# Optimization experiments

Hardware: AMD Instinct MI355X
Metric: run time of the kernel (lower is better)

The kernel has to match this reference:

```python
import jax, jax.numpy as jnp
import numpy as np

N_NODES = 50000
N_EDGES = 800000
N_GRAPHS = 512
NEG_SLOPE = 0.2  # PyG GATConv default LeakyReLU slope


def _gat_layer(x, src, dst, W, a_src, a_dst, b, n_nodes):
    """PyG-style GATConv (concat=True, self-loops already in src/dst)."""
    H, C = a_src.shape
    h = (x @ W).reshape(n_nodes, H, C)            # [N, H, C]
    e_s = (h * a_src).sum(-1)                     # [N, H]
    e_d = (h * a_dst).sum(-1)                     # [N, H]
    e = jax.nn.leaky_relu(e_s[src] + e_d[dst], NEG_SLOPE)  # [E, H]
    # segment softmax over destination nodes
    m = jax.ops.segment_max(e, dst, num_segments=n_nodes)
    w = jnp.exp(e - m[dst])
    s = jax.ops.segment_sum(w, dst, num_segments=n_nodes)
    alpha = w / (s[dst] + 1e-16)                  # [E, H]
    out = jax.ops.segment_sum(h[src] * alpha[:, :, None], dst, num_segments=n_nodes)
    return out.reshape(n_nodes, H * C) + b


def setup_inputs() -> dict:
    key = jax.random.key(0)
    ks = jax.random.split(key, 16)
    x = jax.random.normal(ks[0], (N_NODES, 2), dtype=jnp.float32)
    edge_index = jax.random.randint(ks[1], (2, N_EDGES), 0, N_NODES, dtype=jnp.int64 if jax.config.jax_enable_x64 else jnp.int32)
    batch = jnp.sort(jax.random.randint(ks[2], (N_NODES,), 0, N_GRAPHS))
    g = lambda k, shape: (jax.random.normal(k, shape, dtype=jnp.float32) * 0.1)
    return {
        "x": x, "edge_index": edge_index, "batch": batch,
        "W1": g(ks[3], (2, 64)),   "a1s": g(ks[4], (8, 8)),  "a1d": g(ks[5], (8, 8)),  "b1": jnp.zeros((64,), jnp.float32),
        "W2": g(ks[6], (64, 128)), "a2s": g(ks[7], (8, 16)), "a2d": g(ks[8], (8, 16)), "b2": jnp.zeros((128,), jnp.float32),
        "W3": g(ks[9], (128, 128)),"a3s": g(ks[10], (8, 16)),"a3d": g(ks[11], (8, 16)),"b3": jnp.zeros((128,), jnp.float32),
        "fc1W": g(ks[12], (128, 32)), "fc1b": jnp.zeros((32,), jnp.float32),
        "fc2W": g(ks[13], (32, 10)),  "fc2b": jnp.zeros((10,), jnp.float32),
    }


def reference(x, edge_index, batch, W1, a1s, a1d, b1, W2, a2s, a2d, b2, W3, a3s, a3d, b3, fc1W, fc1b, fc2W, fc2b):
    n = x.shape[0]
    loop = jnp.arange(n, dtype=edge_index.dtype)
    src = jnp.concatenate([edge_index[0], loop])  # add self-loops (PyG default)
    dst = jnp.concatenate([edge_index[1], loop])
    h = jax.nn.elu(_gat_layer(x, src, dst, W1, a1s, a1d, b1, n))
    h = jax.nn.elu(_gat_layer(h, src, dst, W2, a2s, a2d, b2, n))
    h = _gat_layer(h, src, dst, W3, a3s, a3d, b3, n)
    # global mean pool over graphs
    sums = jax.ops.segment_sum(h, batch, num_segments=N_GRAPHS)
    cnt = jax.ops.segment_sum(jnp.ones((n,), h.dtype), batch, num_segments=N_GRAPHS)
    pooled = sums / jnp.maximum(cnt, 1.0)[:, None]   # [G, 128]
    z = jax.nn.relu(pooled @ fc1W + fc1b)
    return jax.nn.log_softmax(z @ fc2W + fc2b, axis=1)
```

## Files before the change

### kernel.cpp

```cpp
#include <hip/hip_runtime.h>
#include <cstddef>
#include <cstdint>

typedef __attribute__((ext_vector_type(8))) short bf16x8;
typedef __attribute__((ext_vector_type(4))) float floatx4;
typedef __attribute__((ext_vector_type(2))) float v2f;

#define BSTRIDE 8192


__device__ __forceinline__ unsigned bf16pair(float a, float b) {
    unsigned ua = __float_as_uint(a), ub = __float_as_uint(b);
    ua += 0x7fffu + ((ua >> 16) & 1u);
    ub += 0x7fffu + ((ub >> 16) & 1u);
    return (ua >> 16) | (ub & 0xffff0000u);
}
__device__ __forceinline__ unsigned short bf16one(float a) {
    unsigned ua = __float_as_uint(a);
    ua += 0x7fffu + ((ua >> 16) & 1u);
    return (unsigned short)(ua >> 16);
}


__global__ __launch_bounds__(256) void prep_k(
    const int* __restrict__ edge, unsigned* __restrict__ barr,
    int* __restrict__ bcnt, int E, int EA, int B1,
    const float* __restrict__ W2, unsigned short* __restrict__ Wt2,
    const float* __restrict__ W3, unsigned short* __restrict__ Wt3,
    const float* __restrict__ x, const float* __restrict__ W1,
    const float* __restrict__ a1s, const float* __restrict__ a1d,
    unsigned char* __restrict__ h8a, float* __restrict__ es,
    float* __restrict__ ed, int N) {
    int tid = threadIdx.x;
    if ((int)blockIdx.x < B1) {
        __shared__ int h[256];
        __shared__ int lbase[256];
        h[tid] = 0;
        __syncthreads();
        int start = blockIdx.x * 4096;
        unsigned ent[16];
        int lp[16];
#pragma unroll
        for (int k = 0; k < 16; ++k) {
            int i = start + k * 256 + tid;
            if (i < EA) {
                int s, d;
                if (i < E) { s = edge[i]; d = edge[E + i]; }
                else { s = i - E; d = s; }
                int b = d >> 8;
                ent[k] = (unsigned)s | ((unsigned)(d & 255) << 16) | ((unsigned)b << 24);
                lp[k] = atomicAdd(&h[b], 1);
            } else {
                ent[k] = 0xffffffffu;
                lp[k] = 0;
            }
        }
        __syncthreads();
        lbase[tid] = h[tid] ? atomicAdd(&bcnt[tid], h[tid]) : 0;
        __syncthreads();
#pragma unroll
        for (int k = 0; k < 16; ++k) {
            if (ent[k] != 0xffffffffu) {
                int b = ent[k] >> 24;
                int pos = lbase[b] + lp[k];
                if (pos < BSTRIDE)
                    barr[(size_t)b * BSTRIDE + pos] = ent[k] & 0x00ffffffu;
            }
        }
        return;
    }
    if ((int)blockIdx.x < B1 + 96) {
        int rel = blockIdx.x - B1;
        const float* W = (rel < 32) ? W2 : W3;
        unsigned short* Wt = (rel < 32) ? Wt2 : Wt3;
        int total = (rel < 32) ? 8192 : 16384;
        int o = ((rel < 32) ? rel : rel - 32) * 256 + tid;
        if (o < total) {
            int j = o & 7, lane = (o >> 3) & 63, ct = (o >> 9) & 7, ks = o >> 12;
            int k = ks * 32 + (lane >> 4) * 8 + j;
            int n = ct * 16 + (lane & 15);
            Wt[o] = bf16one(W[k * 128 + n]);
        }
        return;
    }
    int wave = tid >> 6, lane = tid & 63;
    int nbase = (blockIdx.x - B1 - 96) * 32;
    float w0 = W1[lane], w1 = W1[64 + lane];
    float as = a1s[lane], ad = a1d[lane];
    int head = lane >> 3;
#pragma unroll
    for (int it = 0; it < 8; ++it) {
        int n = nbase + it * 4 + wave;
        int nc = (n < N) ? n : N - 1;
        float2 xv = ((const float2*)x)[nc];
        float h = xv.x * w0 + xv.y * w1;
        float ps = h * as, pd = h * ad;
#pragma unroll
        for (int off = 1; off < 8; off <<= 1) {
            ps += __shfl_xor(ps, off);
            pd += __shfl_xor(pd, off);
        }
        if (n < N) {
            unsigned d = __builtin_amdgcn_cvt_pk_fp8_f32(h, h, 0, false);
            h8a[(size_t)n * 64 + lane] = (unsigned char)d;
            if ((lane & 7) == 0) { es[n * 8 + head] = ps; ed[n * 8 + head] = pd; }
        }
    }
}


__global__ __launch_bounds__(256) void bucket2_k(const unsigned* __restrict__ barr,
                                                 const int* __restrict__ bcnt,
                                                 int* __restrict__ offsets,
                                                 int* __restrict__ esrc,
                                                 int N, int EA, int nbuck) {
    __shared__ int sd[256];
    __shared__ int bb[256];
    __shared__ int cur[256];
    int b = blockIdx.x, tid = threadIdx.x;
    int v = (tid < nbuck) ? bcnt[tid] : 0;
    sd[tid] = v;
    __syncthreads();
    for (int off = 1; off < 256; off <<= 1) {
        int t = (tid >= off) ? sd[tid - off] : 0;
        __syncthreads();
        sd[tid] += t;
        __syncthreads();
    }
    bb[tid] = sd[tid] - v;
    __syncthreads();
    int bbase = bb[b];
    if (b == 0 && tid == 0) offsets[N] = EA;
    if (b == 0 && tid < 8) esrc[EA + tid] = 0;

    int cnt = bcnt[b];
    const unsigned* arr = barr + (size_t)b * BSTRIDE;
    sd[tid] = 0;
    __syncthreads();
    for (int i = tid; i < cnt; i += 256)
        atomicAdd(&sd[(arr[i] >> 16) & 0xff], 1);
    __syncthreads();
    v = sd[tid];
    for (int off = 1; off < 256; off <<= 1) {
        int t = (tid >= off) ? sd[tid - off] : 0;
        __syncthreads();
        sd[tid] += t;
        __syncthreads();
    }
    int base = bbase + sd[tid] - v;
    int n = b * 256 + tid;
    if (n < N) offsets[n] = base;
    cur[tid] = base;
    __syncthreads();
    for (int i = tid; i < cnt; i += 256) {
        unsigned e = arr[i];
        int pos = atomicAdd(&cur[(e >> 16) & 0xff], 1);
        esrc[pos] = (int)(e & 0xffffu);
    }
}


template <int IN>
__global__ __launch_bounds__(256) void gemm_mfma_k(
    const unsigned short* __restrict__ a16, const unsigned short* __restrict__ Wt,
    const float* __restrict__ a_s, const float* __restrict__ a_d,
    unsigned char* __restrict__ h8, float* __restrict__ es, float* __restrict__ ed,
    int n_nodes) {
    constexpr int KSTEPS = IN / 32;
    __shared__ float Cl[64 * 132];
    int wave = threadIdx.x >> 6, lane = threadIdx.x & 63;
    int q = lane >> 4, m = lane & 15;
    int rbase = blockIdx.x * 64;

    floatx4 acc[8];
#pragma unroll
    for (int ct = 0; ct < 8; ++ct) acc[ct] = (floatx4){0.f, 0.f, 0.f, 0.f};

    int ra = rbase + wave * 16 + m;
    if (ra >= n_nodes) ra = n_nodes - 1;
    const unsigned short* arow = a16 + (size_t)ra * IN + q * 8;

#pragma unroll
    for (int ks = 0; ks < KSTEPS; ++ks) {
        bf16x8 af = *(const bf16x8*)(arow + ks * 32);
        const unsigned short* wp = Wt + ((size_t)(ks * 8) * 64 + lane) * 8;
#pragma unroll
        for (int ct = 0; ct < 8; ++ct) {
            bf16x8 bf = *(const bf16x8*)(wp + (size_t)ct * 64 * 8);
            acc[ct] = __builtin_amdgcn_mfma_f32_16x16x32_bf16(af, bf, acc[ct], 0, 0, 0);
        }
    }

#pragma unroll
    for (int ct = 0; ct < 8; ++ct)
#pragma unroll
        for (int i = 0; i < 4; ++i)
            Cl[(wave * 16 + q * 4 + i) * 132 + ct * 16 + m] = acc[ct][i];
    __syncthreads();

    int rl = threadIdx.x >> 2, part = threadIdx.x & 3;
    int r = rbase + rl;
    if (r < n_nodes) {
        const float* cp = &Cl[rl * 132 + part * 32];
        float e0s = 0.f, e0d = 0.f, e1s = 0.f, e1d = 0.f;
#pragma unroll
        for (int c = 0; c < 16; ++c) {
            float v = cp[c];
            int ai = part * 32 + c;
            e0s += v * a_s[ai];
            e0d += v * a_d[ai];
        }
#pragma unroll
        for (int c = 16; c < 32; ++c) {
            float v = cp[c];
            int ai = part * 32 + c;
            e1s += v * a_s[ai];
            e1d += v * a_d[ai];
        }
        unsigned pk8[8];
#pragma unroll
        for (int u = 0; u < 8; ++u) {
            unsigned d = __builtin_amdgcn_cvt_pk_fp8_f32(cp[4 * u], cp[4 * u + 1], 0, false);
            d = __builtin_amdgcn_cvt_pk_fp8_f32(cp[4 * u + 2], cp[4 * u + 3], d, true);
            pk8[u] = d;
        }
        uint4* hp = (uint4*)(h8 + (size_t)r * 128) + part * 2;
        hp[0] = make_uint4(pk8[0], pk8[1], pk8[2], pk8[3]);
        hp[1] = make_uint4(pk8[4], pk8[5], pk8[6], pk8[7]);
        es[r * 8 + 2 * part] = e0s;
        es[r * 8 + 2 * part + 1] = e1s;
        ed[r * 8 + 2 * part] = e0d;
        ed[r * 8 + 2 * part + 1] = e1d;
    }
}


template <int NCOL, bool ELU, bool POOL>
__global__ __launch_bounds__(256) void gat_k(
    const unsigned char* __restrict__ hsrc, const float* __restrict__ es,
    const float* __restrict__ ed, const int* __restrict__ offsets,
    const int* __restrict__ esrc, const float* __restrict__ bias,
    void* __restrict__ outp, const int* __restrict__ batch,
    float* __restrict__ sums, float* __restrict__ cnt, int n_nodes) {
    constexpr int UPL = NCOL / 16;
    __shared__ float vbuf[POOL ? 8 * 128 : 1];
    int wave = threadIdx.x >> 6, lane = threadIdx.x & 63;
    int half = lane >> 5;
    int hl = lane & 31;
    int slot = hl >> 3;
    int l = lane & 7;
    int ni = wave * 2 + half;
    int n = blockIdx.x * 8 + ni;
    bool valid = (n < n_nodes);
    int nc = valid ? n : 0;
    float edn = ed[nc * 8 + l];
    int start = valid ? offsets[nc] : 0;
    int end = valid ? offsets[nc + 1] : 0;

    v2f acc2[UPL];
#pragma unroll
    for (int k = 0; k < UPL; ++k) acc2[k] = (v2f){0.f, 0.f};
    float s = 0.f;

    for (int j = start; j < end; j += 4) {
        int jj = j + slot;
        bool act = (jj < end);
        int src = esrc[jj];
        float e0 = es[(size_t)src * 8 + l] + edn;
        float e = fmaxf(e0, 0.2f * e0);
        float p = act ? __expf(e) : 0.f;
        s += p;
        v2f p2 = (v2f){p, p};
        if constexpr (NCOL == 128) {
            uint4 u = *(const uint4*)(hsrc + (size_t)src * 128 + 16 * l);
            acc2[0] += p2 * (v2f)__builtin_amdgcn_cvt_pk_f32_fp8(u.x, false);
            acc2[1] += p2 * (v2f)__builtin_amdgcn_cvt_pk_f32_fp8(u.x, true);
            acc2[2] += p2 * (v2f)__builtin_amdgcn_cvt_pk_f32_fp8(u.y, false);
            acc2[3] += p2 * (v2f)__builtin_amdgcn_cvt_pk_f32_fp8(u.y, true);
            acc2[4] += p2 * (v2f)__builtin_amdgcn_cvt_pk_f32_fp8(u.z, false);
            acc2[5] += p2 * (v2f)__builtin_amdgcn_cvt_pk_f32_fp8(u.z, true);
            acc2[6] += p2 * (v2f)__builtin_amdgcn_cvt_pk_f32_fp8(u.w, false);
            acc2[7] += p2 * (v2f)__builtin_amdgcn_cvt_pk_f32_fp8(u.w, true);
        } else {
            uint2 u = *(const uint2*)(hsrc + (size_t)src * 64 + 8 * l);
            acc2[0] += p2 * (v2f)__builtin_amdgcn_cvt_pk_f32_fp8(u.x, false);
            acc2[1] += p2 * (v2f)__builtin_amdgcn_cvt_pk_f32_fp8(u.x, true);
            acc2[2] += p2 * (v2f)__builtin_amdgcn_cvt_pk_f32_fp8(u.y, false);
            acc2[3] += p2 * (v2f)__builtin_amdgcn_cvt_pk_f32_fp8(u.y, true);
        }
    }

    s += __shfl_xor(s, 8);
    s += __shfl_xor(s, 16);
    float v[2 * UPL];
#pragma unroll
    for (int k = 0; k < UPL; ++k) { v[2 * k] = acc2[k].x; v[2 * k + 1] = acc2[k].y; }
#pragma unroll
    for (int k = 0; k < 2 * UPL; ++k) {
        v[k] += __shfl_xor(v[k], 8);
        v[k] += __shfl_xor(v[k], 16);
    }

    if (slot == 0 && valid) {
        float r = 1.f / (s + 1e-16f);
#pragma unroll
        for (int k = 0; k < 2 * UPL; ++k) {
            float b = bias[(2 * UPL) * l + k];
            float t = v[k] * r + b;
            if constexpr (ELU) t = (t > 0.f) ? t : expm1f(t);
            v[k] = t;
        }
        if constexpr (POOL) {
#pragma unroll
            for (int k = 0; k < 2 * UPL; ++k)
                vbuf[ni * 128 + (2 * UPL) * l + k] = v[k];
        } else if constexpr (NCOL == 128) {
            uint4* op = (uint4*)outp + (size_t)n * 16 + 2 * l;
            op[0] = make_uint4(bf16pair(v[0], v[1]), bf16pair(v[2], v[3]),
                               bf16pair(v[4], v[5]), bf16pair(v[6], v[7]));
            op[1] = make_uint4(bf16pair(v[8], v[9]), bf16pair(v[10], v[11]),
                               bf16pair(v[12], v[13]), bf16pair(v[14], v[15]));
        } else {
            ((uint4*)outp)[(size_t)n * 8 + l] =
                make_uint4(bf16pair(v[0], v[1]), bf16pair(v[2], v[3]),
                           bf16pair(v[4], v[5]), bf16pair(v[6], v[7]));
        }
    }

    if constexpr (POOL) {
        __syncthreads();
        int c = threadIdx.x;
        if (c < 128) {
            float acc = 0.f, cacc = 0.f;
            int gprev = -1;
            for (int k = 0; k < 8; ++k) {
                int nn = blockIdx.x * 8 + k;
                if (nn >= n_nodes) break;
                int g = batch[nn];
                if (g != gprev) {
                    if (gprev >= 0) {
                        atomicAdd(&sums[gprev * 128 + c], acc);
                        if (c == 0) atomicAdd(&cnt[gprev], cacc);
                    }
                    acc = 0.f; cacc = 0.f; gprev = g;
                }
                acc += vbuf[k * 128 + c];
                cacc += 1.f;
            }
            if (gprev >= 0) {
                atomicAdd(&sums[gprev * 128 + c], acc);
                if (c == 0) atomicAdd(&cnt[gprev], cacc);
            }
        }
    }
}


__global__ __launch_bounds__(64) void fc_k(const float* __restrict__ sums,
                                           const float* __restrict__ cnt,
                                           const float* __restrict__ fc1W,
                                           const float* __restrict__ fc1b,
                                           const float* __restrict__ fc2W,
                                           const float* __restrict__ fc2b,
                                           float* __restrict__ out) {
    int g = blockIdx.x, lane = threadIdx.x;
    __shared__ float p[128];
    __shared__ float z[32];
    __shared__ float logits[10];
    float inv = 1.f / fmaxf(cnt[g], 1.f);
    p[lane] = sums[g * 128 + lane] * inv;
    p[lane + 64] = sums[g * 128 + 64 + lane] * inv;
    __syncthreads();
    if (lane < 32) {
        float a = fc1b[lane];
        for (int k = 0; k < 128; k++) a += p[k] * fc1W[k * 32 + lane];
        z[lane] = fmaxf(a, 0.f);
    }
    __syncthreads();
    if (lane < 10) {
        float a = fc2b[lane];
        for (int k = 0; k < 32; k++) a += z[k] * fc2W[k * 10 + lane];
        logits[lane] = a;
    }
    __syncthreads();
    if (lane < 10) {
        float mx = logits[0];
#pragma unroll
        for (int i = 1; i < 10; i++) mx = fmaxf(mx, logits[i]);
        float se = 0.f;
#pragma unroll
        for (int i = 0; i < 10; i++) se += __expf(logits[i] - mx);
        out[g * 10 + lane] = logits[lane] - mx - logf(se);
    }
}


extern "C" void kernel_launch(void* const* d_in, const int* in_sizes, int n_in,
                              void* d_out, int out_size, void* d_ws, size_t ws_size,
                              hipStream_t stream) {
    const float* x = (const float*)d_in[0];
    const int* edge = (const int*)d_in[1];
    const int* batch = (const int*)d_in[2];
    const float* W1 = (const float*)d_in[3];
    const float* a1s = (const float*)d_in[4];
    const float* a1d = (const float*)d_in[5];
    const float* b1 = (const float*)d_in[6];
    const float* W2 = (const float*)d_in[7];
    const float* a2s = (const float*)d_in[8];
    const float* a2d = (const float*)d_in[9];
    const float* b2 = (const float*)d_in[10];
    const float* W3 = (const float*)d_in[11];
    const float* a3s = (const float*)d_in[12];
    const float* a3d = (const float*)d_in[13];
    const float* b3 = (const float*)d_in[14];
    const float* fc1W = (const float*)d_in[15];
    const float* fc1b = (const float*)d_in[16];
    const float* fc2W = (const float*)d_in[17];
    const float* fc2b = (const float*)d_in[18];
    float* out = (float*)d_out;

    const int N = in_sizes[0] / 2;
    const int E = in_sizes[1] / 2;
    const int EA = E + N;
    const int NG = out_size / 10;
    const int NBUCK = (N + 255) >> 8;
    const int B1 = (EA + 4095) / 4096;
    const int G1 = (N + 31) / 32;

    char* p = (char*)d_ws;
    unsigned char* h8 = (unsigned char*)p; p += (size_t)N * 128;
    unsigned char* h8a = (unsigned char*)p; p += (size_t)N * 64;
    unsigned short* a16a = (unsigned short*)p; p += (size_t)N * 64 * 2;
    unsigned short* a16b = (unsigned short*)p; p += (size_t)N * 128 * 2;
    unsigned short* Wt2 = (unsigned short*)p; p += (size_t)64 * 128 * 2;
    unsigned short* Wt3 = (unsigned short*)p; p += (size_t)128 * 128 * 2;
    float* es = (float*)p;  p += (size_t)N * 8 * 4;
    float* ed = (float*)p;  p += (size_t)N * 8 * 4;
    float* sums = (float*)p; p += (size_t)NG * 128 * 4;
    float* cnt = (float*)p;  p += (size_t)NG * 4;
    int* bcnt = (int*)p;     p += 256 * 4;
    int* offsets = (int*)p;  p += (size_t)(N + 1) * 4;
    int* esrc = (int*)p;     p += (size_t)(EA + 8) * 4;
    unsigned* barr = (unsigned*)p; p += (size_t)NBUCK * BSTRIDE * 4;

    hipMemsetAsync(sums, 0, ((size_t)NG * 128 + NG + 256) * 4, stream);

    prep_k<<<B1 + 96 + G1, 256, 0, stream>>>(
        edge, barr, bcnt, E, EA, B1, W2, Wt2, W3, Wt3,
        x, W1, a1s, a1d, h8a, es, ed, N);
    bucket2_k<<<NBUCK, 256, 0, stream>>>(barr, bcnt, offsets, esrc, N, EA, NBUCK);

    int mblocks = (N + 63) / 64;
    int ablocks = (N + 7) / 8;
    gat_k<64, true, false><<<ablocks, 256, 0, stream>>>(
        h8a, es, ed, offsets, esrc, b1, a16a, batch, sums, cnt, N);
    gemm_mfma_k<64><<<mblocks, 256, 0, stream>>>(a16a, Wt2, a2s, a2d, h8, es, ed, N);
    gat_k<128, true, false><<<ablocks, 256, 0, stream>>>(
        h8, es, ed, offsets, esrc, b2, a16b, batch, sums, cnt, N);
    gemm_mfma_k<128><<<mblocks, 256, 0, stream>>>(a16b, Wt3, a3s, a3d, h8, es, ed, N);
    gat_k<128, false, true><<<ablocks, 256, 0, stream>>>(
        h8, es, ed, offsets, esrc, b3, nullptr, batch, sums, cnt, N);

    fc_k<<<NG, 64, 0, stream>>>(sums, cnt, fc1W, fc1b, fc2W, fc2b, out);
}
```

Baseline: 271.6 us.

## Fuse GAT aggregation with next-layer MFMA projection into one kernel

```diff
diff --git a/kernel.cpp b/kernel.cpp
--- a/kernel.cpp
+++ b/kernel.cpp
@@ -160,25 +160,111 @@
 }
 
 
-template <int IN>
-__global__ __launch_bounds__(256) void gemm_mfma_k(
-    const unsigned short* __restrict__ a16, const unsigned short* __restrict__ Wt,
+template <int NCOL, bool ELU>
+__global__ __launch_bounds__(256) void gatmfma_k(
+    const unsigned char* __restrict__ hsrc, const float* __restrict__ es_in,
+    const float* __restrict__ ed_in, const int* __restrict__ offsets,
+    const int* __restrict__ esrc, const float* __restrict__ bias,
+    unsigned short* __restrict__ a16, const unsigned short* __restrict__ Wt,
     const float* __restrict__ a_s, const float* __restrict__ a_d,
-    unsigned char* __restrict__ h8, float* __restrict__ es, float* __restrict__ ed,
-    int n_nodes) {
-    constexpr int KSTEPS = IN / 32;
+    unsigned char* __restrict__ h8_out, float* __restrict__ es_out,
+    float* __restrict__ ed_out, int n_nodes) {
+    constexpr int UPL = NCOL / 16;
     __shared__ float Cl[64 * 132];
     int wave = threadIdx.x >> 6, lane = threadIdx.x & 63;
+    int rbase = blockIdx.x * 64;
+
+    int half = lane >> 5;
+    int hl = lane & 31;
+    int slot = hl >> 3;
+    int l = lane & 7;
+    for (int pass = 0; pass < 8; ++pass) {
+        int n = rbase + pass * 8 + wave * 2 + half;
+        bool valid = (n < n_nodes);
+        int nc = valid ? n : 0;
+        float edn = ed_in[nc * 8 + l];
+        int start = valid ? offsets[nc] : 0;
+        int end = valid ? offsets[nc + 1] : 0;
+
+        v2f acc2[UPL];
+#pragma unroll
+        for (int k = 0; k < UPL; ++k) acc2[k] = (v2f){0.f, 0.f};
+        float s = 0.f;
+
+        for (int j = start; j < end; j += 4) {
+            int jj = j + slot;
+            bool act = (jj < end);
+            int src = esrc[jj];
+            float e0 = es_in[(size_t)src * 8 + l] + edn;
+            float e = fmaxf(e0, 0.2f * e0);
+            float p = act ? __expf(e) : 0.f;
+            s += p;
+            v2f p2 = (v2f){p, p};
+            if constexpr (NCOL == 128) {
+                uint4 u = *(const uint4*)(hsrc + (size_t)src * 128 + 16 * l);
+                acc2[0] += p2 * (v2f)__builtin_amdgcn_cvt_pk_f32_fp8(u.x, false);
+                acc2[1] += p2 * (v2f)__builtin_amdgcn_cvt_pk_f32_fp8(u.x, true);
+                acc2[2] += p2 * (v2f)__builtin_amdgcn_cvt_pk_f32_fp8(u.y, false);
+                acc2[3] += p2 * (v2f)__builtin_amdgcn_cvt_pk_f32_fp8(u.y, true);
+                acc2[4] += p2 * (v2f)__builtin_amdgcn_cvt_pk_f32_fp8(u.z, false);
+                acc2[5] += p2 * (v2f)__builtin_amdgcn_cvt_pk_f32_fp8(u.z, true);
+                acc2[6] += p2 * (v2f)__builtin_amdgcn_cvt_pk_f32_fp8(u.w, false);
+                acc2[7] += p2 * (v2f)__builtin_amdgcn_cvt_pk_f32_fp8(u.w, true);
+            } else {
+                uint2 u = *(const uint2*)(hsrc + (size_t)src * 64 + 8 * l);
+                acc2[0] += p2 * (v2f)__builtin_amdgcn_cvt_pk_f32_fp8(u.x, false);
+                acc2[1] += p2 * (v2f)__builtin_amdgcn_cvt_pk_f32_fp8(u.x, true);
+                acc2[2] += p2 * (v2f)__builtin_amdgcn_cvt_pk_f32_fp8(u.y, false);
+                acc2[3] += p2 * (v2f)__builtin_amdgcn_cvt_pk_f32_fp8(u.y, true);
+            }
+        }
+
+        s += __shfl_xor(s, 8);
+        s += __shfl_xor(s, 16);
+        float v[2 * UPL];
+#pragma unroll
+        for (int k = 0; k < UPL; ++k) { v[2 * k] = acc2[k].x; v[2 * k + 1] = acc2[k].y; }
+#pragma unroll
+        for (int k = 0; k < 2 * UPL; ++k) {
+            v[k] += __shfl_xor(v[k], 8);
+            v[k] += __shfl_xor(v[k], 16);
+        }
+
+        if (slot == 0 && valid) {
+            float r = 1.f / (s + 1e-16f);
+#pragma unroll
+            for (int k = 0; k < 2 * UPL; ++k) {
+                float b = bias[(2 * UPL) * l + k];
+                float t = v[k] * r + b;
+                if constexpr (ELU) t = (t > 0.f) ? t : expm1f(t);
+                v[k] = t;
+            }
+            if constexpr (NCOL == 128) {
+                uint4* op = (uint4*)a16 + (size_t)n * 16 + 2 * l;
+                op[0] = make_uint4(bf16pair(v[0], v[1]), bf16pair(v[2], v[3]),
+                                   bf16pair(v[4], v[5]), bf16pair(v[6], v[7]));
+                op[1] = make_uint4(bf16pair(v[8], v[9]), bf16pair(v[10], v[11]),
+                                   bf16pair(v[12], v[13]), bf16pair(v[14], v[15]));
+            } else {
+                ((uint4*)a16)[(size_t)n * 8 + l] =
+                    make_uint4(bf16pair(v[0], v[1]), bf16pair(v[2], v[3]),
+                               bf16pair(v[4], v[5]), bf16pair(v[6], v[7]));
+            }
+        }
+    }
+
+    __threadfence_block();
+    __syncthreads();
+
+    constexpr int KSTEPS = NCOL / 32;
     int q = lane >> 4, m = lane & 15;
-    int rbase = blockIdx.x * 64;
-
     floatx4 acc[8];
 #pragma unroll
     for (int ct = 0; ct < 8; ++ct) acc[ct] = (floatx4){0.f, 0.f, 0.f, 0.f};
 
     int ra = rbase + wave * 16 + m;
     if (ra >= n_nodes) ra = n_nodes - 1;
-    const unsigned short* arow = a16 + (size_t)ra * IN + q * 8;
+    const unsigned short* arow = a16 + (size_t)ra * NCOL + q * 8;
 
 #pragma unroll
     for (int ks = 0; ks < KSTEPS; ++ks) {
@@ -205,17 +291,17 @@
         float e0s = 0.f, e0d = 0.f, e1s = 0.f, e1d = 0.f;
 #pragma unroll
         for (int c = 0; c < 16; ++c) {
-            float v = cp[c];
+            float vv = cp[c];
             int ai = part * 32 + c;
-            e0s += v * a_s[ai];
-            e0d += v * a_d[ai];
+            e0s += vv * a_s[ai];
+            e0d += vv * a_d[ai];
         }
 #pragma unroll
         for (int c = 16; c < 32; ++c) {
-            float v = cp[c];
+            float vv = cp[c];
             int ai = part * 32 + c;
-            e1s += v * a_s[ai];
-            e1d += v * a_d[ai];
+            e1s += vv * a_s[ai];
+            e1d += vv * a_d[ai];
         }
         unsigned pk8[8];
 #pragma unroll
@@ -224,26 +310,25 @@
             d = __builtin_amdgcn_cvt_pk_fp8_f32(cp[4 * u + 2], cp[4 * u + 3], d, true);
             pk8[u] = d;
         }
-        uint4* hp = (uint4*)(h8 + (size_t)r * 128) + part * 2;
+        uint4* hp = (uint4*)(h8_out + (size_t)r * 128) + part * 2;
         hp[0] = make_uint4(pk8[0], pk8[1], pk8[2], pk8[3]);
         hp[1] = make_uint4(pk8[4], pk8[5], pk8[6], pk8[7]);
-        es[r * 8 + 2 * part] = e0s;
-        es[r * 8 + 2 * part + 1] = e1s;
-        ed[r * 8 + 2 * part] = e0d;
-        ed[r * 8 + 2 * part + 1] = e1d;
-    }
-}
-
-
-template <int NCOL, bool ELU, bool POOL>
-__global__ __launch_bounds__(256) void gat_k(
+        es_out[r * 8 + 2 * part] = e0s;
+        es_out[r * 8 + 2 * part + 1] = e1s;
+        ed_out[r * 8 + 2 * part] = e0d;
+        ed_out[r * 8 + 2 * part + 1] = e1d;
+    }
+}
+
+
+__global__ __launch_bounds__(256) void gatpool_k(
     const unsigned char* __restrict__ hsrc, const float* __restrict__ es,
     const float* __restrict__ ed, const int* __restrict__ offsets,
     const int* __restrict__ esrc, const float* __restrict__ bias,
-    void* __restrict__ outp, const int* __restrict__ batch,
-    float* __restrict__ sums, float* __restrict__ cnt, int n_nodes) {
-    constexpr int UPL = NCOL / 16;
-    __shared__ float vbuf[POOL ? 8 * 128 : 1];
+    const int* __restrict__ batch, float* __restrict__ sums,
+    float* __restrict__ cnt, int n_nodes) {
+    constexpr int UPL = 8;
+    __shared__ float vbuf[8 * 128];
     int wave = threadIdx.x >> 6, lane = threadIdx.x & 63;
     int half = lane >> 5;
     int hl = lane & 31;
@@ -271,32 +356,24 @@
         float p = act ? __expf(e) : 0.f;
         s += p;
         v2f p2 = (v2f){p, p};
-        if constexpr (NCOL == 128) {
-            uint4 u = *(const uint4*)(hsrc + (size_t)src * 128 + 16 * l);
-            acc2[0] += p2 * (v2f)__builtin_amdgcn_cvt_pk_f32_fp8(u.x, false);
-            acc2[1] += p2 * (v2f)__builtin_amdgcn_cvt_pk_f32_fp8(u.x, true);
-            acc2[2] += p2 * (v2f)__builtin_amdgcn_cvt_pk_f32_fp8(u.y, false);
-            acc2[3] += p2 * (v2f)__builtin_amdgcn_cvt_pk_f32_fp8(u.y, true);
-            acc2[4] += p2 * (v2f)__builtin_amdgcn_cvt_pk_f32_fp8(u.z, false);
-            acc2[5] += p2 * (v2f)__builtin_amdgcn_cvt_pk_f32_fp8(u.z, true);
-            acc2[6] += p2 * (v2f)__builtin_amdgcn_cvt_pk_f32_fp8(u.w, false);
-            acc2[7] += p2 * (v2f)__builtin_amdgcn_cvt_pk_f32_fp8(u.w, true);
-        } else {
-            uint2 u = *(const uint2*)(hsrc + (size_t)src * 64 + 8 * l);
-            acc2[0] += p2 * (v2f)__builtin_amdgcn_cvt_pk_f32_fp8(u.x, false);
-            acc2[1] += p2 * (v2f)__builtin_amdgcn_cvt_pk_f32_fp8(u.x, true);
-            acc2[2] += p2 * (v2f)__builtin_amdgcn_cvt_pk_f32_fp8(u.y, false);
-            acc2[3] += p2 * (v2f)__builtin_amdgcn_cvt_pk_f32_fp8(u.y, true);
-        }
+        uint4 u = *(const uint4*)(hsrc + (size_t)src * 128 + 16 * l);
+        acc2[0] += p2 * (v2f)__builtin_amdgcn_cvt_pk_f32_fp8(u.x, false);
+        acc2[1] += p2 * (v2f)__builtin_amdgcn_cvt_pk_f32_fp8(u.x, true);
+        acc2[2] += p2 * (v2f)__builtin_amdgcn_cvt_pk_f32_fp8(u.y, false);
+        acc2[3] += p2 * (v2f)__builtin_amdgcn_cvt_pk_f32_fp8(u.y, true);
+        acc2[4] += p2 * (v2f)__builtin_amdgcn_cvt_pk_f32_fp8(u.z, false);
+        acc2[5] += p2 * (v2f)__builtin_amdgcn_cvt_pk_f32_fp8(u.z, true);
+        acc2[6] += p2 * (v2f)__builtin_amdgcn_cvt_pk_f32_fp8(u.w, false);
+        acc2[7] += p2 * (v2f)__builtin_amdgcn_cvt_pk_f32_fp8(u.w, true);
     }
 
     s += __shfl_xor(s, 8);
     s += __shfl_xor(s, 16);
-    float v[2 * UPL];
+    float v[16];
 #pragma unroll
     for (int k = 0; k < UPL; ++k) { v[2 * k] = acc2[k].x; v[2 * k + 1] = acc2[k].y; }
 #pragma unroll
-    for (int k = 0; k < 2 * UPL; ++k) {
+    for (int k = 0; k < 16; ++k) {
         v[k] += __shfl_xor(v[k], 8);
         v[k] += __shfl_xor(v[k], 16);
     }
@@ -304,53 +381,32 @@
     if (slot == 0 && valid) {
         float r = 1.f / (s + 1e-16f);
 #pragma unroll
-        for (int k = 0; k < 2 * UPL; ++k) {
-            float b = bias[(2 * UPL) * l + k];
-            float t = v[k] * r + b;
-            if constexpr (ELU) t = (t > 0.f) ? t : expm1f(t);
-            v[k] = t;
-        }
-        if constexpr (POOL) {
-#pragma unroll
-            for (int k = 0; k < 2 * UPL; ++k)
-                vbuf[ni * 128 + (2 * UPL) * l + k] = v[k];
-        } else if constexpr (NCOL == 128) {
-            uint4* op = (uint4*)outp + (size_t)n * 16 + 2 * l;
-            op[0] = make_uint4(bf16pair(v[0], v[1]), bf16pair(v[2], v[3]),
-                               bf16pair(v[4], v[5]), bf16pair(v[6], v[7]));
-            op[1] = make_uint4(bf16pair(v[8], v[9]), bf16pair(v[10], v[11]),
-                               bf16pair(v[12], v[13]), bf16pair(v[14], v[15]));
-        } else {
-            ((uint4*)outp)[(size_t)n * 8 + l] =
-                make_uint4(bf16pair(v[0], v[1]), bf16pair(v[2], v[3]),
-                           bf16pair(v[4], v[5]), bf16pair(v[6], v[7]));
-        }
-    }
-
-    if constexpr (POOL) {
-        __syncthreads();
-        int c = threadIdx.x;
-        if (c < 128) {
-            float acc = 0.f, cacc = 0.f;
-            int gprev = -1;
-            for (int k = 0; k < 8; ++k) {
-                int nn = blockIdx.x * 8 + k;
-                if (nn >= n_nodes) break;
-                int g = batch[nn];
-                if (g != gprev) {
-                    if (gprev >= 0) {
-                        atomicAdd(&sums[gprev * 128 + c], acc);
-                        if (c == 0) atomicAdd(&cnt[gprev], cacc);
-                    }
-                    acc = 0.f; cacc = 0.f; gprev = g;
+        for (int k = 0; k < 16; ++k)
+            vbuf[ni * 128 + 16 * l + k] = v[k] * r + bias[16 * l + k];
+    }
+
+    __syncthreads();
+    int c = threadIdx.x;
+    if (c < 128) {
+        float acc = 0.f, cacc = 0.f;
+        int gprev = -1;
+        for (int k = 0; k < 8; ++k) {
+            int nn = blockIdx.x * 8 + k;
+            if (nn >= n_nodes) break;
+            int g = batch[nn];
+            if (g != gprev) {
+                if (gprev >= 0) {
+                    atomicAdd(&sums[gprev * 128 + c], acc);
+                    if (c == 0) atomicAdd(&cnt[gprev], cacc);
                 }
-                acc += vbuf[k * 128 + c];
-                cacc += 1.f;
+                acc = 0.f; cacc = 0.f; gprev = g;
             }
-            if (gprev >= 0) {
-                atomicAdd(&sums[gprev * 128 + c], acc);
-                if (c == 0) atomicAdd(&cnt[gprev], cacc);
-            }
+            acc += vbuf[k * 128 + c];
+            cacc += 1.f;
+        }
+        if (gprev >= 0) {
+            atomicAdd(&sums[gprev * 128 + c], acc);
+            if (c == 0) atomicAdd(&cnt[gprev], cacc);
         }
     }
 }
@@ -428,14 +484,20 @@
     const int G1 = (N + 31) / 32;
 
     char* p = (char*)d_ws;
-    unsigned char* h8 = (unsigned char*)p; p += (size_t)N * 128;
-    unsigned char* h8a = (unsigned char*)p; p += (size_t)N * 64;
+    unsigned char* h8b = (unsigned char*)p; p += (size_t)N * 128;
+    unsigned char* h8a = (unsigned char*)p;
+    unsigned char* h8c = (unsigned char*)p;
+    p += (size_t)N * 64;
     unsigned short* a16a = (unsigned short*)p; p += (size_t)N * 64 * 2;
     unsigned short* a16b = (unsigned short*)p; p += (size_t)N * 128 * 2;
     unsigned short* Wt2 = (unsigned short*)p; p += (size_t)64 * 128 * 2;
     unsigned short* Wt3 = (unsigned short*)p; p += (size_t)128 * 128 * 2;
-    float* es = (float*)p;  p += (size_t)N * 8 * 4;
-    float* ed = (float*)p;  p += (size_t)N * 8 * 4;
+    float* esa = (float*)p; p += (size_t)N * 8 * 4;
+    float* eda = (float*)p; p += (size_t)N * 8 * 4;
+    float* esb = (float*)p; p += (size_t)N * 8 * 4;
+    float* edb = (float*)p; p += (size_t)N * 8 * 4;
+    float* esc = esa;
+    float* edc = eda;
     float* sums = (float*)p; p += (size_t)NG * 128 * 4;
     float* cnt = (float*)p;  p += (size_t)NG * 4;
     int* bcnt = (int*)p;     p += 256 * 4;
@@ -447,19 +509,16 @@
 
     prep_k<<<B1 + 96 + G1, 256, 0, stream>>>(
         edge, barr, bcnt, E, EA, B1, W2, Wt2, W3, Wt3,
-        x, W1, a1s, a1d, h8a, es, ed, N);
+        x, W1, a1s, a1d, h8a, esa, eda, N);
     bucket2_k<<<NBUCK, 256, 0, stream>>>(barr, bcnt, offsets, esrc, N, EA, NBUCK);
 
-    int mblocks = (N + 63) / 64;
-    int ablocks = (N + 7) / 8;
-    gat_k<64, true, false><<<ablocks, 256, 0, stream>>>(
-        h8a, es, ed, offsets, esrc, b1, a16a, batch, sums, cnt, N);
-    gemm_mfma_k<64><<<mblocks, 256, 0, stream>>>(a16a, Wt2, a2s, a2d, h8, es, ed, N);
-    gat_k<128, true, false><<<ablocks, 256, 0, stream>>>(
-        h8, es, ed, offsets, esrc, b2, a16b, batch, sums, cnt, N);
-    gemm_mfma_k<128><<<mblocks, 256, 0, stream>>>(a16b, Wt3, a3s, a3d, h8, es, ed, N);
-    gat_k<128, false, true><<<ablocks, 256, 0, stream>>>(
-        h8, es, ed, offsets, esrc, b3, nullptr, batch, sums, cnt, N);
+    int fblocks = (N + 63) / 64;
+    gatmfma_k<64, true><<<fblocks, 256, 0, stream>>>(
+        h8a, esa, eda, offsets, esrc, b1, a16a, Wt2, a2s, a2d, h8b, esb, edb, N);
+    gatmfma_k<128, true><<<fblocks, 256, 0, stream>>>(
+        h8b, esb, edb, offsets, esrc, b2, a16b, Wt3, a3s, a3d, h8c, esc, edc, N);
+    gatpool_k<<<(N + 7) / 8, 256, 0, stream>>>(
+        h8c, esc, edc, offsets, esrc, b3, batch, sums, cnt, N);
 
     fc_k<<<NG, 64, 0, stream>>>(sums, cnt, fc1W, fc1b, fc2W, fc2b, out);
 }
```

After: 404.1 us. 48.8% more time.
